# Kernel tuning notes

Measured on AMD Instinct MI355X. Metric: run time of the kernel, lower is better.

The kernel has to match this reference:

```python
import jax, jax.numpy as jnp
import numpy as np

N, E, R, D = 50000, 100000, 64, 50


def setup_inputs() -> dict:
    key = jax.random.key(0)
    k0, k1, k2, k3, k4 = jax.random.split(key, 5)
    h = jax.random.normal(k0, (N, D), dtype=jnp.float32)
    # xavier_uniform with gain=sqrt(2) (relu): bound = gain*sqrt(6/(fan_in+fan_out))
    bound = np.sqrt(2.0) * np.sqrt(6.0 / (D + D))
    weight = jax.random.uniform(k1, (R, D, D), dtype=jnp.float32, minval=-bound, maxval=bound)
    bias = jnp.ones((D,), dtype=jnp.float32)
    src_idx = jax.random.randint(k2, (E,), 0, N)
    dst_idx = jax.random.randint(k3, (E,), 0, N)
    rel_type = jax.random.randint(k4, (E,), 0, R)
    return {"h": h, "weight": weight, "bias": bias,
            "src_idx": src_idx, "dst_idx": dst_idx, "rel_type": rel_type}


def reference(h, weight, bias, src_idx, dst_idx, rel_type):
    # message_func: per-edge relation weight gather + bmm with source features
    # h[src_idx]: [E, D], weight[rel_type]: [E, D, D] -> msg: [E, D]
    msg = jnp.einsum('ed,edk->ek', h[src_idx], weight[rel_type])
    # sum-reduce messages onto destination nodes (DGL fn.sum semantics)
    agg = jax.ops.segment_sum(msg, dst_idx, num_segments=N)
    # apply_func: bias add + ReLU on node features
    return jax.nn.relu(agg + bias)
```

## Files before the change

### kernel.cpp

```cpp
#include <hip/hip_runtime.h>

#define NN 50000
#define DD 50
#define RR 64
#define SUBS 32
#define BINS (RR * SUBS)
#define CAP 128
#define GPB (CAP / 16)
#define SLOTS (BINS * CAP)
#define WLMAX 8192
#define CAPN 24
#define MSGROWS (WLMAX * 16)
#define MSTRIDE 50

#define BINCUR_OFF 0
#define WL_OFF     2048
#define DCUR_OFF   10240
#define PERM_OFF   60240
#define SD_OFF     1260240
#define META_INTS  1784528
#define WB_BYTE    ((size_t)META_INTS * 4)
#define MSG_BYTE   (WB_BYTE + (size_t)RR * 64 * 64 * 2)
#define WS_NEED    (MSG_BYTE + (size_t)MSGROWS * MSTRIDE * 4)

typedef __attribute__((ext_vector_type(8))) short bf16x8;
typedef __attribute__((ext_vector_type(4))) float f32x4;

__device__ __forceinline__ unsigned short f2b(float f) {
    unsigned u = __float_as_uint(f);
    u = (u + 0x7fffu + ((u >> 16) & 1u)) >> 16;
    return (unsigned short)u;
}

__global__ void init_kernel(float4* __restrict__ out4, int n4, int* __restrict__ meta,
                            unsigned short* __restrict__ wb, const float* __restrict__ w,
                            int zero_out) {
    int i = blockIdx.x * blockDim.x + threadIdx.x;
    int stride = gridDim.x * blockDim.x;
    if (zero_out) for (int j = i; j < n4; j += stride) out4[j] = make_float4(0.f, 0.f, 0.f, 0.f);
    if (i < BINS) meta[BINCUR_OFF + i] = i * CAP;
    if (i < WLMAX) meta[WL_OFF + i] = -1;
    for (int j = i; j < NN; j += stride) meta[DCUR_OFF + j] = j * CAPN;
    for (int j = i; j < RR * 64 * 64; j += stride) {
        int r = j >> 12, d = (j >> 6) & 63, n = j & 63;
        float v = (n < DD && d < DD) ? w[r * (DD * DD) + d * DD + n] : 0.f;
        wb[(r << 12) + (n << 6) + d] = f2b(v);
    }
}

__global__ void scatter_kernel(const int* __restrict__ src, const int* __restrict__ dst,
                               const int* __restrict__ rel, int E, int* __restrict__ meta) {
    int e = blockIdx.x * blockDim.x + threadIdx.x;
    if (e >= E) return;
    int sb = (rel[e] << 5) | (e & 31);
    int p = atomicAdd(&meta[BINCUR_OFF + sb], 1);
    if (p < (sb + 1) * CAP)
        ((int2*)(meta + SD_OFF))[p] = make_int2(src[e], dst[e]);
}

__global__ __launch_bounds__(1024) void compact_kernel(int* __restrict__ meta) {
    __shared__ int ws1[16];
    int tid = threadIdx.x, lane = tid & 63, wv = tid >> 6;
    int b0 = tid * 2, b1 = b0 + 1;
    int c0 = meta[BINCUR_OFF + b0] - b0 * CAP; c0 = c0 < 0 ? 0 : (c0 > CAP ? CAP : c0);
    int c1 = meta[BINCUR_OFF + b1] - b1 * CAP; c1 = c1 < 0 ? 0 : (c1 > CAP ? CAP : c1);
    int ng0 = (c0 + 15) >> 4, ng1 = (c1 + 15) >> 4, ng = ng0 + ng1;
    int x = ng;
    #pragma unroll
    for (int d = 1; d < 64; d <<= 1) { int y = __shfl_up(x, d); if (lane >= d) x += y; }
    if (lane == 63) ws1[wv] = x;
    __syncthreads();
    if (tid == 0) { int cum = 0; for (int i = 0; i < 16; ++i) { int v = ws1[i]; ws1[i] = cum; cum += v; } }
    __syncthreads();
    int off = ws1[wv] + x - ng;
    for (int gi = 0; gi < ng0; ++gi) {
        int nv = c0 - gi * 16; nv = nv > 16 ? 16 : nv;
        meta[WL_OFF + off + gi] = ((b0 * GPB + gi) << 5) | nv;
    }
    off += ng0;
    for (int gi = 0; gi < ng1; ++gi) {
        int nv = c1 - gi * 16; nv = nv > 16 ? 16 : nv;
        meta[WL_OFF + off + gi] = ((b1 * GPB + gi) << 5) | nv;
    }
}

template<int MODE>
__global__ __launch_bounds__(256) void edge_kernel(const float* __restrict__ h,
                                                   const unsigned short* __restrict__ wb,
                                                   int* __restrict__ meta,
                                                   float* __restrict__ dstbuf) {
    int lane = threadIdx.x & 63;
    int widx = __builtin_amdgcn_readfirstlane((blockIdx.x << 2) + (threadIdx.x >> 6));
    int entry = meta[WL_OFF + widx];
    if (entry < 0) return;
    entry = __builtin_amdgcn_readfirstlane(entry);
    int nv = entry & 31;
    int g  = entry >> 5;
    int sb = g >> 3;
    int gi = g & (GPB - 1);
    int r  = sb >> 5;
    int base = sb * CAP + gi * 16;

    int sv0 = 0, dv0 = -1;
    if (lane < nv) {
        int2 sd = ((const int2*)(meta + SD_OFF))[base + lane];
        sv0 = sd.x; dv0 = sd.y;
    }
    if (MODE == 1 && lane < nv) {
        int pos = atomicAdd(&meta[DCUR_OFF + dv0], 1);
        if (pos < (dv0 + 1) * CAPN)
            meta[PERM_OFF + pos] = (widx << 4) + lane;
    }
    int sv = __shfl(sv0, lane & 15);
    int ch = lane >> 4;

    const float* __restrict__ hrow = h + (size_t)sv * DD;
    const float2* hp0 = (const float2*)(hrow + ch * 8);
    float2 q0 = hp0[0], q1 = hp0[1], q2 = hp0[2], q3 = hp0[3];
    int kb = 32 + ch * 8;
    const float2 z2 = make_float2(0.f, 0.f);
    float2 q4 = (kb + 1 < DD) ? *(const float2*)(hrow + kb)     : z2;
    float2 q5 = (kb + 3 < DD) ? *(const float2*)(hrow + kb + 2) : z2;
    float2 q6 = (kb + 5 < DD) ? *(const float2*)(hrow + kb + 4) : z2;
    float2 q7 = (kb + 7 < DD) ? *(const float2*)(hrow + kb + 6) : z2;

    bf16x8 a0, a1;
    a0[0] = f2b(q0.x); a0[1] = f2b(q0.y); a0[2] = f2b(q1.x); a0[3] = f2b(q1.y);
    a0[4] = f2b(q2.x); a0[5] = f2b(q2.y); a0[6] = f2b(q3.x); a0[7] = f2b(q3.y);
    a1[0] = f2b(q4.x); a1[1] = f2b(q4.y); a1[2] = f2b(q5.x); a1[3] = f2b(q5.y);
    a1[4] = f2b(q6.x); a1[5] = f2b(q6.y); a1[6] = f2b(q7.x); a1[7] = f2b(q7.y);

    const unsigned short* wr = wb + ((size_t)r << 12) + ((lane & 15) << 6) + (ch << 3);
    f32x4 c[4];
    #pragma unroll
    for (int t = 0; t < 4; ++t) c[t] = (f32x4){0.f, 0.f, 0.f, 0.f};
    #pragma unroll
    for (int t = 0; t < 4; ++t) {
        bf16x8 b0 = *(const bf16x8*)(wr + t * 1024);
        bf16x8 b1 = *(const bf16x8*)(wr + t * 1024 + 32);
        c[t] = __builtin_amdgcn_mfma_f32_16x16x32_bf16(a0, b0, c[t], 0, 0, 0);
        c[t] = __builtin_amdgcn_mfma_f32_16x16x32_bf16(a1, b1, c[t], 0, 0, 0);
    }

    int col0 = lane & 15;
    if (MODE == 1) {
        float* mb = dstbuf + (size_t)((widx << 4) + (ch << 2)) * MSTRIDE;
        #pragma unroll
        for (int q = 0; q < 4; ++q)
            #pragma unroll
            for (int t = 0; t < 4; ++t) {
                int col = t * 16 + col0;
                if (col < DD) mb[q * MSTRIDE + col] = c[t][q];
            }
    } else {
        #pragma unroll
        for (int q = 0; q < 4; ++q) {
            int rw = ch * 4 + q;
            int dq = __shfl(dv0, rw);
            if (dq >= 0) {
                float* op = dstbuf + (size_t)dq * DD;
                #pragma unroll
                for (int t = 0; t < 4; ++t) {
                    int col = t * 16 + col0;
                    if (col < DD) atomicAdd(op + col, c[t][q]);
                }
            }
        }
    }
}

__global__ __launch_bounds__(256) void agg_kernel(const float* __restrict__ msg,
                                                  const int* __restrict__ meta,
                                                  const float* __restrict__ bias,
                                                  float* __restrict__ out) {
    int lane = threadIdx.x & 63;
    int n = __builtin_amdgcn_readfirstlane((blockIdx.x << 2) + (threadIdx.x >> 6));
    if (n >= NN) return;
    int cnt = meta[DCUR_OFF + n] - n * CAPN;
    if (cnt > CAPN) cnt = CAPN;
    float v = 0.f;
    for (int j = 0; j < cnt; ++j) {
        int p = meta[PERM_OFF + n * CAPN + j];
        if (lane < DD) v += msg[(size_t)p * MSTRIDE + lane];
    }
    if (lane < DD) {
        float o = v + bias[lane];
        out[(size_t)n * DD + lane] = o > 0.f ? o : 0.f;
    }
}

__global__ void finalize_kernel(float* __restrict__ out, const float* __restrict__ bias, int total2) {
    int i = blockIdx.x * blockDim.x + threadIdx.x;
    if (i < total2) {
        float2 v = ((float2*)out)[i];
        int p = (i * 2) % DD;
        v.x += bias[p];
        v.y += bias[p + 1];
        v.x = v.x > 0.f ? v.x : 0.f;
        v.y = v.y > 0.f ? v.y : 0.f;
        ((float2*)out)[i] = v;
    }
}

extern "C" void kernel_launch(void* const* d_in, const int* in_sizes, int n_in,
                              void* d_out, int out_size, void* d_ws, size_t ws_size,
                              hipStream_t stream) {
    const float* h      = (const float*)d_in[0];
    const float* weight = (const float*)d_in[1];
    const float* bias   = (const float*)d_in[2];
    const int*   src    = (const int*)d_in[3];
    const int*   dst    = (const int*)d_in[4];
    const int*   rel    = (const int*)d_in[5];
    float* out = (float*)d_out;
    int*   meta = (int*)d_ws;
    unsigned short* wb = (unsigned short*)((char*)d_ws + WB_BYTE);

    const int E = in_sizes[3];
    const bool big = ws_size >= WS_NEED;

    init_kernel<<<2048, 256, 0, stream>>>((float4*)out, out_size / 4, meta, wb, weight, big ? 0 : 1);
    scatter_kernel<<<(E + 255) / 256, 256, 0, stream>>>(src, dst, rel, E, meta);
    compact_kernel<<<1, 1024, 0, stream>>>(meta);
    if (big) {
        float* msg = (float*)((char*)d_ws + MSG_BYTE);
        edge_kernel<1><<<WLMAX / 4, 256, 0, stream>>>(h, wb, meta, msg);
        agg_kernel<<<(NN + 3) / 4, 256, 0, stream>>>(msg, meta, bias, out);
    } else {
        edge_kernel<0><<<WLMAX / 4, 256, 0, stream>>>(h, wb, meta, out);
        int total2 = out_size / 2;
        finalize_kernel<<<(total2 + 255) / 256, 256, 0, stream>>>(out, bias, total2);
    }
}
```

Baseline: 64.37 us.

## Pre-convert node features to padded bf16 and store messages in bf16

Node features are converted once in the init kernel into a 64-wide padded bf16 table, so the edge kernel loads two 16-byte vectors per row instead of strided float2 loads followed by per-element conversion. Per-edge messages are now written as bf16 with a 64-column stride, and the aggregation kernel loads all permutation indices with vector loads and runs an unrolled loop over them. This trades an extra full pass over h (50000 rows) in init, plus added rounding of messages to bf16, for less memory traffic in the edge and aggregation stages. In the small-workspace path, hb and msg still point into the workspace, which may not be large enough to hold them.

Measured after the change: 65.62 us. About the same (+1.9%).

```diff
diff --git a/kernel.cpp b/kernel.cpp
--- a/kernel.cpp
+++ b/kernel.cpp
@@ -11,7 +11,6 @@
 #define WLMAX 8192
 #define CAPN 24
 #define MSGROWS (WLMAX * 16)
-#define MSTRIDE 50
 
 #define BINCUR_OFF 0
 #define WL_OFF     2048
@@ -20,8 +19,9 @@
 #define SD_OFF     1260240
 #define META_INTS  1784528
 #define WB_BYTE    ((size_t)META_INTS * 4)
-#define MSG_BYTE   (WB_BYTE + (size_t)RR * 64 * 64 * 2)
-#define WS_NEED    (MSG_BYTE + (size_t)MSGROWS * MSTRIDE * 4)
+#define HB_BYTE    (WB_BYTE + (size_t)RR * 64 * 64 * 2)
+#define MSG_BYTE   (HB_BYTE + (size_t)NN * 64 * 2)
+#define WS_NEED    (MSG_BYTE + (size_t)MSGROWS * 64 * 2)
 
 typedef __attribute__((ext_vector_type(8))) short bf16x8;
 typedef __attribute__((ext_vector_type(4))) float f32x4;
@@ -33,7 +33,8 @@
 }
 
 __global__ void init_kernel(float4* __restrict__ out4, int n4, int* __restrict__ meta,
-                            unsigned short* __restrict__ wb, const float* __restrict__ w,
+                            unsigned short* __restrict__ wb, unsigned short* __restrict__ hb,
+                            const float* __restrict__ w, const float* __restrict__ h,
                             int zero_out) {
     int i = blockIdx.x * blockDim.x + threadIdx.x;
     int stride = gridDim.x * blockDim.x;
@@ -46,6 +47,10 @@
         float v = (n < DD && d < DD) ? w[r * (DD * DD) + d * DD + n] : 0.f;
         wb[(r << 12) + (n << 6) + d] = f2b(v);
     }
+    for (int j = i; j < NN * 64; j += stride) {
+        int n = j >> 6, c = j & 63;
+        hb[j] = (c < DD) ? f2b(h[n * DD + c]) : (unsigned short)0;
+    }
 }
 
 __global__ void scatter_kernel(const int* __restrict__ src, const int* __restrict__ dst,
@@ -85,10 +90,11 @@
 }
 
 template<int MODE>
-__global__ __launch_bounds__(256) void edge_kernel(const float* __restrict__ h,
+__global__ __launch_bounds__(256) void edge_kernel(const unsigned short* __restrict__ hb,
                                                    const unsigned short* __restrict__ wb,
                                                    int* __restrict__ meta,
-                                                   float* __restrict__ dstbuf) {
+                                                   float* __restrict__ outbuf,
+                                                   unsigned short* __restrict__ msg) {
     int lane = threadIdx.x & 63;
     int widx = __builtin_amdgcn_readfirstlane((blockIdx.x << 2) + (threadIdx.x >> 6));
     int entry = meta[WL_OFF + widx];
@@ -114,21 +120,9 @@
     int sv = __shfl(sv0, lane & 15);
     int ch = lane >> 4;
 
-    const float* __restrict__ hrow = h + (size_t)sv * DD;
-    const float2* hp0 = (const float2*)(hrow + ch * 8);
-    float2 q0 = hp0[0], q1 = hp0[1], q2 = hp0[2], q3 = hp0[3];
-    int kb = 32 + ch * 8;
-    const float2 z2 = make_float2(0.f, 0.f);
-    float2 q4 = (kb + 1 < DD) ? *(const float2*)(hrow + kb)     : z2;
-    float2 q5 = (kb + 3 < DD) ? *(const float2*)(hrow + kb + 2) : z2;
-    float2 q6 = (kb + 5 < DD) ? *(const float2*)(hrow + kb + 4) : z2;
-    float2 q7 = (kb + 7 < DD) ? *(const float2*)(hrow + kb + 6) : z2;
-
-    bf16x8 a0, a1;
-    a0[0] = f2b(q0.x); a0[1] = f2b(q0.y); a0[2] = f2b(q1.x); a0[3] = f2b(q1.y);
-    a0[4] = f2b(q2.x); a0[5] = f2b(q2.y); a0[6] = f2b(q3.x); a0[7] = f2b(q3.y);
-    a1[0] = f2b(q4.x); a1[1] = f2b(q4.y); a1[2] = f2b(q5.x); a1[3] = f2b(q5.y);
-    a1[4] = f2b(q6.x); a1[5] = f2b(q6.y); a1[6] = f2b(q7.x); a1[7] = f2b(q7.y);
+    const unsigned short* hrow = hb + ((size_t)sv << 6) + (ch << 3);
+    bf16x8 a0 = *(const bf16x8*)hrow;
+    bf16x8 a1 = *(const bf16x8*)(hrow + 32);
 
     const unsigned short* wr = wb + ((size_t)r << 12) + ((lane & 15) << 6) + (ch << 3);
     f32x4 c[4];
@@ -144,21 +138,19 @@
 
     int col0 = lane & 15;
     if (MODE == 1) {
-        float* mb = dstbuf + (size_t)((widx << 4) + (ch << 2)) * MSTRIDE;
+        unsigned short* mb = msg + (size_t)((widx << 4) + (ch << 2)) * 64;
         #pragma unroll
         for (int q = 0; q < 4; ++q)
             #pragma unroll
-            for (int t = 0; t < 4; ++t) {
-                int col = t * 16 + col0;
-                if (col < DD) mb[q * MSTRIDE + col] = c[t][q];
-            }
+            for (int t = 0; t < 4; ++t)
+                mb[q * 64 + t * 16 + col0] = f2b(c[t][q]);
     } else {
         #pragma unroll
         for (int q = 0; q < 4; ++q) {
             int rw = ch * 4 + q;
             int dq = __shfl(dv0, rw);
             if (dq >= 0) {
-                float* op = dstbuf + (size_t)dq * DD;
+                float* op = outbuf + (size_t)dq * DD;
                 #pragma unroll
                 for (int t = 0; t < 4; ++t) {
                     int col = t * 16 + col0;
@@ -169,7 +161,7 @@
     }
 }
 
-__global__ __launch_bounds__(256) void agg_kernel(const float* __restrict__ msg,
+__global__ __launch_bounds__(256) void agg_kernel(const unsigned short* __restrict__ msg,
                                                   const int* __restrict__ meta,
                                                   const float* __restrict__ bias,
                                                   float* __restrict__ out) {
@@ -178,10 +170,18 @@
     if (n >= NN) return;
     int cnt = meta[DCUR_OFF + n] - n * CAPN;
     if (cnt > CAPN) cnt = CAPN;
+    const int4* pp = (const int4*)(meta + PERM_OFF + n * CAPN);
+    int4 P0 = pp[0], P1 = pp[1], P2 = pp[2], P3 = pp[3], P4 = pp[4], P5 = pp[5];
+    int pj[CAPN] = {P0.x, P0.y, P0.z, P0.w, P1.x, P1.y, P1.z, P1.w,
+                    P2.x, P2.y, P2.z, P2.w, P3.x, P3.y, P3.z, P3.w,
+                    P4.x, P4.y, P4.z, P4.w, P5.x, P5.y, P5.z, P5.w};
     float v = 0.f;
-    for (int j = 0; j < cnt; ++j) {
-        int p = meta[PERM_OFF + n * CAPN + j];
-        if (lane < DD) v += msg[(size_t)p * MSTRIDE + lane];
+    #pragma unroll
+    for (int j = 0; j < CAPN; ++j) {
+        if (j < cnt) {
+            unsigned short u = msg[(size_t)pj[j] * 64 + lane];
+            v += __uint_as_float((unsigned)u << 16);
+        }
     }
     if (lane < DD) {
         float o = v + bias[lane];
@@ -213,20 +213,22 @@
     const int*   rel    = (const int*)d_in[5];
     float* out = (float*)d_out;
     int*   meta = (int*)d_ws;
-    unsigned short* wb = (unsigned short*)((char*)d_ws + WB_BYTE);
+    unsigned short* wb  = (unsigned short*)((char*)d_ws + WB_BYTE);
+    unsigned short* hb  = (unsigned short*)((char*)d_ws + HB_BYTE);
+    unsigned short* msg = (unsigned short*)((char*)d_ws + MSG_BYTE);
 
     const int E = in_sizes[3];
     const bool big = ws_size >= WS_NEED;
 
-    init_kernel<<<2048, 256, 0, stream>>>((float4*)out, out_size / 4, meta, wb, weight, big ? 0 : 1);
+    init_kernel<<<2048, 256, 0, stream>>>((float4*)out, out_size / 4, meta, wb, hb, weight, h,
+                                          big ? 0 : 1);
     scatter_kernel<<<(E + 255) / 256, 256, 0, stream>>>(src, dst, rel, E, meta);
     compact_kernel<<<1, 1024, 0, stream>>>(meta);
     if (big) {
-        float* msg = (float*)((char*)d_ws + MSG_BYTE);
-        edge_kernel<1><<<WLMAX / 4, 256, 0, stream>>>(h, wb, meta, msg);
+        edge_kernel<1><<<WLMAX / 4, 256, 0, stream>>>(hb, wb, meta, out, msg);
         agg_kernel<<<(NN + 3) / 4, 256, 0, stream>>>(msg, meta, bias, out);
     } else {
-        edge_kernel<0><<<WLMAX / 4, 256, 0, stream>>>(h, wb, meta, out);
+        edge_kernel<0><<<WLMAX / 4, 256, 0, stream>>>(hb, wb, meta, out, msg);
         int total2 = out_size / 2;
         finalize_kernel<<<(total2 + 255) / 256, 256, 0, stream>>>(out, bias, total2);
     }
```
